# Kernel tuning notes

Measured on AMD Instinct MI355X. Metric: run time of the kernel, lower is better.

Reference implementation:

```python
import jax, jax.numpy as jnp
import numpy as np

DIM, D_STATE, D_CONV, EXPAND = 512, 16, 4, 2
D_INNER = EXPAND * DIM            # 1024
DT_RANK = (DIM + 15) // 16        # 32
B, L = 2, 2048


def setup_inputs() -> dict:
    key = jax.random.key(0)
    ks = jax.random.split(key, 12)
    s_in = 1.0 / np.sqrt(DIM)
    s_xp = 1.0 / np.sqrt(D_INNER)
    s_dt = 1.0 / np.sqrt(DT_RANK)
    return {
        "x": jax.random.normal(ks[0], (B, L, DIM), jnp.float32),
        "ln_g": jnp.ones((DIM,), jnp.float32),
        "ln_b": jnp.zeros((DIM,), jnp.float32),
        "W_in": jax.random.normal(ks[1], (2 * D_INNER, DIM), jnp.float32) * s_in,
        "conv_w": jax.random.normal(ks[2], (D_INNER, D_CONV), jnp.float32) * 0.5,
        "conv_b": jax.random.normal(ks[3], (D_INNER,), jnp.float32) * 0.1,
        "W_xproj": jax.random.normal(ks[4], (DT_RANK + 2 * D_STATE, D_INNER), jnp.float32) * s_xp,
        "W_dt": jax.random.normal(ks[5], (D_INNER, DT_RANK), jnp.float32) * s_dt,
        "b_dt": jax.random.normal(ks[6], (D_INNER,), jnp.float32) * 0.1 - 4.0,  # softplus -> small dt
        "A_log": jnp.log(jax.random.uniform(ks[7], (D_INNER, D_STATE), jnp.float32, 1.0, 16.0)),
        "Dp": jax.random.normal(ks[8], (D_INNER,), jnp.float32),
        "W_out": jax.random.normal(ks[9], (DIM, D_INNER), jnp.float32) * s_xp,
    }


def _layernorm(x, g, b, eps=1e-5):
    mu = jnp.mean(x, -1, keepdims=True)
    var = jnp.mean(jnp.square(x - mu), -1, keepdims=True)
    return (x - mu) * jax.lax.rsqrt(var + eps) * g + b


def reference(x, ln_g, ln_b, W_in, conv_w, conv_b, W_xproj, W_dt, b_dt, A_log, Dp, W_out):
    h = _layernorm(x, ln_g, ln_b)
    # input projection -> [B,L,2*d_inner]
    xz = jnp.einsum('bld,ed->ble', h, W_in)
    xp, z = jnp.split(xz, 2, axis=-1)
    # depthwise causal conv1d over time (kernel d_conv), then SiLU
    xp_pad = jnp.pad(xp, ((0, 0), (D_CONV - 1, 0), (0, 0)))
    xc = conv_b
    for k in range(D_CONV):
        xc = xc + xp_pad[:, k:k + L, :] * conv_w[:, k]
    xc = jax.nn.silu(xc)
    # x_proj -> dt, B, C
    proj = jnp.einsum('bld,ed->ble', xc, W_xproj)
    dt_r = proj[..., :DT_RANK]
    Bm = proj[..., DT_RANK:DT_RANK + D_STATE]          # [B,L,n]
    Cm = proj[..., DT_RANK + D_STATE:]                 # [B,L,n]
    dt = jax.nn.softplus(jnp.einsum('blr,dr->bld', dt_r, W_dt) + b_dt)  # [B,L,d]
    A = -jnp.exp(A_log)                                # [d,n]
    dA = jnp.exp(jnp.einsum('bld,dn->bldn', dt, A))    # [B,L,d,n]
    dBx = dt[..., None] * Bm[:, :, None, :] * xc[..., None]  # [B,L,d,n]
    # selective scan over time (time-major for lax.scan)
    def step(s, inp):
        dA_t, dBx_t, C_t = inp
        s = s * dA_t + dBx_t                           # [B,d,n]
        y_t = jnp.einsum('bdn,bn->bd', s, C_t)
        return s, y_t
    s0 = jnp.zeros((B, D_INNER, D_STATE), xc.dtype)
    _, ys = jax.lax.scan(step, s0,
                         (jnp.moveaxis(dA, 1, 0), jnp.moveaxis(dBx, 1, 0), jnp.moveaxis(Cm, 1, 0)))
    y = jnp.moveaxis(ys, 0, 1)                         # [B,L,d]
    y = y + xc * Dp
    y = y * jax.nn.silu(z)
    out = jnp.einsum('bld,ed->ble', y, W_out)
    return x + out  # dropout is identity in eval mode
```

## Files before the change

### kernel.cpp

```cpp
#include <hip/hip_runtime.h>
#include <hip/hip_bf16.h>
#include <math.h>

#define B_      2
#define L_      2048
#define DIM_    512
#define DINNER  1024
#define DTRANK  32
#define DSTATE  16
#define DCONV   4
#define BL      (B_ * L_)
#define NCHUNK  128
#define CBITS   7
#define CLEN    (L_ / NCHUNK)

typedef __attribute__((ext_vector_type(8))) short bf16x8;
typedef __attribute__((ext_vector_type(4))) float f32x4;

static __device__ __forceinline__ unsigned short f2bf(float f) {
  __hip_bfloat16 h = __float2bfloat16(f);
  return *(unsigned short*)&h;
}
static __device__ __forceinline__ float bf2f(unsigned short u) {
  return __uint_as_float(((unsigned int)u) << 16);
}

static __device__ __forceinline__ void gload16(const void* g, void* l) {
  __builtin_amdgcn_global_load_lds(
      (const __attribute__((address_space(1))) void*)g,
      (__attribute__((address_space(3))) void*)l, 16, 0, 0);
}

static __device__ __forceinline__ float softplus_f(float acc) {
  return (acc > 20.f) ? acc : __logf(1.f + __expf(acc));
}

__global__ __launch_bounds__(256) void cvt_ln_kernel(
    const float* __restrict__ s0, const float* __restrict__ s1,
    const float* __restrict__ s2, __hip_bfloat16* __restrict__ d0,
    __hip_bfloat16* __restrict__ d1, __hip_bfloat16* __restrict__ d2,
    const float* __restrict__ x, const float* __restrict__ g,
    const float* __restrict__ b, __hip_bfloat16* __restrict__ h) {
  int blk = blockIdx.x;
  if (blk < 1600) {
    int i = (blk * 256 + threadIdx.x) * 4;
    const float* s; __hip_bfloat16* d; int off;
    if (i < 1048576)            { s = s0; d = d0; off = i; }
    else if (i < 1048576+65536) { s = s1; d = d1; off = i - 1048576; }
    else                        { s = s2; d = d2; off = i - 1114112; }
    float4 v = *(const float4*)(s + off);
    d[off + 0] = __float2bfloat16(v.x);
    d[off + 1] = __float2bfloat16(v.y);
    d[off + 2] = __float2bfloat16(v.z);
    d[off + 3] = __float2bfloat16(v.w);
    return;
  }
  int row = (blk - 1600) * 4 + (threadIdx.x >> 6);
  int lane = threadIdx.x & 63;
  const float* xr = x + (size_t)row * DIM_;
  float v[8];
  float sum = 0.f;
#pragma unroll
  for (int i = 0; i < 8; i++) { v[i] = xr[lane + i * 64]; sum += v[i]; }
#pragma unroll
  for (int o = 32; o > 0; o >>= 1) sum += __shfl_xor(sum, o, 64);
  float mu = sum * (1.f / DIM_);
  float vs = 0.f;
#pragma unroll
  for (int i = 0; i < 8; i++) { float dd = v[i] - mu; vs += dd * dd; }
#pragma unroll
  for (int o = 32; o > 0; o >>= 1) vs += __shfl_xor(vs, o, 64);
  float rstd = rsqrtf(vs * (1.f / DIM_) + 1e-5f);
  __hip_bfloat16* hr = h + (size_t)row * DIM_;
#pragma unroll
  for (int i = 0; i < 8; i++) {
    int c = lane + i * 64;
    hr[c] = __float2bfloat16((v[i] - mu) * rstd * g[c] + b[c]);
  }
}

template <bool ADD_RES, bool OUT_BF16>
__global__ __launch_bounds__(256) void gemm_mfma_128(
    const __hip_bfloat16* __restrict__ A, int lda,
    const __hip_bfloat16* __restrict__ Bw, int ldb,
    const float* __restrict__ Res, int ldr,
    void* __restrict__ C, int ldc, int K) {
  __shared__ short As[128 * 64];
  __shared__ short Bs[128 * 64];
  int t = threadIdx.x;
  int n0 = blockIdx.x * 128, m0 = blockIdx.y * 128;
  int w = t >> 6, lane = t & 63;
  int wm = (w >> 1) * 64, wn = (w & 1) * 64;
  int l15 = lane & 15, quad = lane >> 4;
  int lr = lane >> 3, lc = (lane & 7) * 8;
  const short* Ag = (const short*)A + (size_t)(m0 + w * 32 + lr) * lda + lc;
  const short* Bg = (const short*)Bw + (size_t)(n0 + w * 32 + lr) * ldb + lc;
  f32x4 acc[4][4];
#pragma unroll
  for (int i = 0; i < 4; i++)
#pragma unroll
    for (int j = 0; j < 4; j++) acc[i][j] = (f32x4){0.f, 0.f, 0.f, 0.f};
  for (int k0 = 0; k0 < K; k0 += 64) {
    __syncthreads();
#pragma unroll
    for (int p = 0; p < 4; p++) {
      gload16(Ag + (size_t)(p * 8) * lda + k0, &As[(w * 32 + p * 8) * 64]);
      gload16(Bg + (size_t)(p * 8) * ldb + k0, &Bs[(w * 32 + p * 8) * 64]);
    }
    __syncthreads();
#pragma unroll
    for (int kk = 0; kk < 64; kk += 32) {
      bf16x8 af[4], bfr[4];
#pragma unroll
      for (int i = 0; i < 4; i++) {
        af[i] = *(const bf16x8*)&As[(wm + i * 16 + l15) * 64 + kk + quad * 8];
        bfr[i] = *(const bf16x8*)&Bs[(wn + i * 16 + l15) * 64 + kk + quad * 8];
      }
#pragma unroll
      for (int i = 0; i < 4; i++)
#pragma unroll
        for (int j = 0; j < 4; j++)
          acc[i][j] = __builtin_amdgcn_mfma_f32_16x16x32_bf16(
              af[i], bfr[j], acc[i][j], 0, 0, 0);
    }
  }
#pragma unroll
  for (int i = 0; i < 4; i++)
#pragma unroll
    for (int r = 0; r < 4; r++) {
      int row = m0 + wm + i * 16 + quad * 4 + r;
#pragma unroll
      for (int j = 0; j < 4; j++) {
        int col = n0 + wn + j * 16 + l15;
        float v = acc[i][j][r];
        if (ADD_RES) v += Res[(size_t)row * ldr + col];
        if (OUT_BF16)
          ((unsigned short*)C)[(size_t)row * ldc + col] = f2bf(v);
        else
          ((float*)C)[(size_t)row * ldc + col] = v;
      }
    }
}

template <bool ADD_RES>
__global__ __launch_bounds__(256) void gemm_mfma_64(
    const __hip_bfloat16* __restrict__ A, int lda,
    const __hip_bfloat16* __restrict__ Bw, int ldb,
    const float* __restrict__ Res, int ldr,
    float* __restrict__ C, int ldc, int K, size_t czs) {
  __shared__ short As[64 * 64];
  __shared__ short Bs[64 * 64];
  int t = threadIdx.x;
  int n0 = blockIdx.x * 64, m0 = blockIdx.y * 64;
  size_t kbase = (size_t)blockIdx.z * K;
  int w = t >> 6, lane = t & 63;
  int wm = (w >> 1) * 32, wn = (w & 1) * 32;
  int l15 = lane & 15, quad = lane >> 4;
  int lr = lane >> 3, lc = (lane & 7) * 8;
  const short* Ag = (const short*)A + (size_t)(m0 + w * 16 + lr) * lda + lc + kbase;
  const short* Bg = (const short*)Bw + (size_t)(n0 + w * 16 + lr) * ldb + lc + kbase;
  f32x4 acc[2][2];
#pragma unroll
  for (int i = 0; i < 2; i++)
#pragma unroll
    for (int j = 0; j < 2; j++) acc[i][j] = (f32x4){0.f, 0.f, 0.f, 0.f};
  for (int k0 = 0; k0 < K; k0 += 64) {
    __syncthreads();
#pragma unroll
    for (int p = 0; p < 2; p++) {
      gload16(Ag + (size_t)(p * 8) * lda + k0, &As[(w * 16 + p * 8) * 64]);
      gload16(Bg + (size_t)(p * 8) * ldb + k0, &Bs[(w * 16 + p * 8) * 64]);
    }
    __syncthreads();
#pragma unroll
    for (int kk = 0; kk < 64; kk += 32) {
      bf16x8 af[2], bfr[2];
#pragma unroll
      for (int i = 0; i < 2; i++) {
        af[i] = *(const bf16x8*)&As[(wm + i * 16 + l15) * 64 + kk + quad * 8];
        bfr[i] = *(const bf16x8*)&Bs[(wn + i * 16 + l15) * 64 + kk + quad * 8];
      }
#pragma unroll
      for (int i = 0; i < 2; i++)
#pragma unroll
        for (int j = 0; j < 2; j++)
          acc[i][j] = __builtin_amdgcn_mfma_f32_16x16x32_bf16(
              af[i], bfr[j], acc[i][j], 0, 0, 0);
    }
  }
  float* Cz = C + czs * blockIdx.z;
#pragma unroll
  for (int i = 0; i < 2; i++)
#pragma unroll
    for (int r = 0; r < 4; r++) {
      int row = m0 + wm + i * 16 + quad * 4 + r;
#pragma unroll
      for (int j = 0; j < 2; j++) {
        int col = n0 + wn + j * 16 + l15;
        float v = acc[i][j][r];
        if (ADD_RES) v += Res[(size_t)row * ldr + col];
        Cz[(size_t)row * ldc + col] = v;
      }
    }
}

__global__ __launch_bounds__(256) void gemm_proj_conv(
    const unsigned short* __restrict__ xzb,
    const __hip_bfloat16* __restrict__ Bw,
    const float* __restrict__ cw, const float* __restrict__ cb,
    __hip_bfloat16* __restrict__ xc_bf,
    float* __restrict__ C, size_t czs) {
  __shared__ short As[64 * 64];
  __shared__ short Bs[64 * 64];
  __shared__ float cws[256 * 4];
  __shared__ float cbs[256];
  int t = threadIdx.x;
  int m0 = blockIdx.y * 64;
  int kbase = blockIdx.z * 256;
  int w = t >> 6, lane = t & 63;
  int wm = (w >> 1) * 32, wn = (w & 1) * 32;
  int l15 = lane & 15, quad = lane >> 4;
  int lrB = lane >> 3, lcB = (lane & 7) * 8;
  const short* Bg = (const short*)Bw + (size_t)(w * 16 + lrB) * DINNER + lcB + kbase;
  *(float4*)&cws[t * 4] = *(const float4*)(cw + (size_t)(kbase + t) * 4);
  cbs[t] = cb[kbase + t];
  int ar = t >> 2, aq = t & 3;
  int bl = m0 + ar;
  int l = bl & (L_ - 1);
  f32x4 acc[2][2];
#pragma unroll
  for (int i = 0; i < 2; i++)
#pragma unroll
    for (int j = 0; j < 2; j++) acc[i][j] = (f32x4){0.f, 0.f, 0.f, 0.f};
  for (int k0 = 0; k0 < 256; k0 += 64) {
    __syncthreads();
#pragma unroll
    for (int p = 0; p < 2; p++)
      gload16(Bg + k0 + (size_t)(p * 8) * DINNER, &Bs[(w * 16 + p * 8) * 64]);
    int dl0 = k0 + aq * 16;
    const unsigned short* xrow = xzb + (size_t)bl * 2048 + kbase + dl0;
    float o[16];
#pragma unroll
    for (int cc = 0; cc < 16; cc++) o[cc] = cbs[dl0 + cc];
#pragma unroll
    for (int k = 0; k < 4; k++) {
      int off = 3 - k;
      bool ok = (l >= off);
      const unsigned short* src = xrow - (size_t)(ok ? off : 0) * 2048;
      bf16x8 v0 = *(const bf16x8*)(src);
      bf16x8 v1 = *(const bf16x8*)(src + 8);
#pragma unroll
      for (int cc = 0; cc < 8; cc++) {
        float xa = ok ? bf2f((unsigned short)v0[cc]) : 0.f;
        float xb = ok ? bf2f((unsigned short)v1[cc]) : 0.f;
        o[cc]     = fmaf(xa, cws[(dl0 + cc) * 4 + k], o[cc]);
        o[cc + 8] = fmaf(xb, cws[(dl0 + cc + 8) * 4 + k], o[cc + 8]);
      }
    }
    bf16x8 pa, pb;
#pragma unroll
    for (int cc = 0; cc < 8; cc++) {
      float va = o[cc] / (1.f + __expf(-o[cc]));
      float vb = o[cc + 8] / (1.f + __expf(-o[cc + 8]));
      pa[cc] = (short)f2bf(va);
      pb[cc] = (short)f2bf(vb);
    }
    *(bf16x8*)&As[ar * 64 + aq * 16] = pa;
    *(bf16x8*)&As[ar * 64 + aq * 16 + 8] = pb;
    unsigned short* xcd = (unsigned short*)xc_bf + (size_t)bl * DINNER + kbase + dl0;
    *(bf16x8*)xcd = pa;
    *(bf16x8*)(xcd + 8) = pb;
    __syncthreads();
#pragma unroll
    for (int kk = 0; kk < 64; kk += 32) {
      bf16x8 af[2], bfr[2];
#pragma unroll
      for (int i = 0; i < 2; i++) {
        af[i] = *(const bf16x8*)&As[(wm + i * 16 + l15) * 64 + kk + quad * 8];
        bfr[i] = *(const bf16x8*)&Bs[(wn + i * 16 + l15) * 64 + kk + quad * 8];
      }
#pragma unroll
      for (int i = 0; i < 2; i++)
#pragma unroll
        for (int j = 0; j < 2; j++)
          acc[i][j] = __builtin_amdgcn_mfma_f32_16x16x32_bf16(
              af[i], bfr[j], acc[i][j], 0, 0, 0);
    }
  }
  float* Cz = C + czs * blockIdx.z;
#pragma unroll
  for (int i = 0; i < 2; i++)
#pragma unroll
    for (int r = 0; r < 4; r++) {
      int row = m0 + wm + i * 16 + quad * 4 + r;
#pragma unroll
      for (int j = 0; j < 2; j++) {
        int col = wn + j * 16 + l15;
        Cz[(size_t)row * 64 + col] = acc[i][j][r];
      }
    }
}

__global__ __launch_bounds__(256) void dt_kernel(
    const float* __restrict__ pp, float* __restrict__ proj,
    const float* __restrict__ Wdt, const float* __restrict__ bdt,
    float* __restrict__ dt) {
  int blk = blockIdx.x;
  int dgrp = blk & 3;
  int bl0 = (blk >> 2) * 8;
  int tid = threadIdx.x;
  int d = dgrp * 256 + tid;
  __shared__ float pr[8 * 64];
  float w[32];
#pragma unroll
  for (int q = 0; q < 8; q++) {
    float4 wv = *(const float4*)(Wdt + (size_t)d * 32 + q * 4);
    w[q * 4 + 0] = wv.x; w[q * 4 + 1] = wv.y;
    w[q * 4 + 2] = wv.z; w[q * 4 + 3] = wv.w;
  }
  float bias = bdt[d];
  if (tid < 128) {
    int o4 = bl0 * 16 + tid;
    float4 v0 = ((const float4*)pp)[o4];
    float4 v1 = ((const float4*)pp)[o4 + 65536];
    float4 v2 = ((const float4*)pp)[o4 + 131072];
    float4 v3 = ((const float4*)pp)[o4 + 196608];
    float4 s;
    s.x = (v0.x + v1.x) + (v2.x + v3.x);
    s.y = (v0.y + v1.y) + (v2.y + v3.y);
    s.z = (v0.z + v1.z) + (v2.z + v3.z);
    s.w = (v0.w + v1.w) + (v2.w + v3.w);
    ((float4*)pr)[tid] = s;
    if (dgrp == 0) *(float4*)(proj + (size_t)bl0 * 64 + tid * 4) = s;
  }
  __syncthreads();
#pragma unroll
  for (int row = 0; row < 8; row++) {
    float a0 = 0.f, a1 = 0.f, a2 = 0.f, a3 = 0.f;
#pragma unroll
    for (int q = 0; q < 8; q++) {
      float4 pv = *(const float4*)&pr[row * 64 + q * 4];
      a0 = fmaf(pv.x, w[q * 4 + 0], a0);
      a1 = fmaf(pv.y, w[q * 4 + 1], a1);
      a2 = fmaf(pv.z, w[q * 4 + 2], a2);
      a3 = fmaf(pv.w, w[q * 4 + 3], a3);
    }
    float acc = bias + ((a0 + a1) + (a2 + a3));
    dt[(size_t)(bl0 + row) * DINNER + d] = softplus_f(acc);
  }
}

__global__ __launch_bounds__(256) void scan1_kernel(
    const float* __restrict__ dt, const __hip_bfloat16* __restrict__ xc_bf,
    const float* __restrict__ proj, const float* __restrict__ A_log,
    float* __restrict__ T, float* __restrict__ E) {
  int bid = blockIdx.x;
  int dgrp4 = bid & 15;
  int c = (bid >> 4) & (NCHUNK - 1);
  int b = bid >> (4 + CBITS);
  int tid = threadIdx.x;
  int dl = tid >> 2;
  int n4 = tid & 3;
  int d0 = dgrp4 * 64;
  int d = d0 + dl;
  int l0 = c * CLEN;
  __shared__ float dts[CLEN * 64];
  __shared__ float xcs[CLEN * 64];
  __shared__ float Bsh[CLEN * 16];
  {
    int row = tid >> 4, c4 = tid & 15;
    *(float4*)&dts[row * 64 + c4 * 4] =
        *(const float4*)(dt + (size_t)(b * L_ + l0 + row) * DINNER + d0 + c4 * 4);
  }
  if (tid < CLEN * 8) {
    int row = tid >> 3, c8 = tid & 7;
    bf16x8 v = *(const bf16x8*)((const unsigned short*)xc_bf +
                                (size_t)(b * L_ + l0 + row) * DINNER + d0 + c8 * 8);
#pragma unroll
    for (int k = 0; k < 8; k++)
      xcs[row * 64 + c8 * 8 + k] = bf2f((unsigned short)v[k]);
  }
  if (tid < CLEN * 4) {
    int row = tid >> 2, c4 = tid & 3;
    *(float4*)&Bsh[row * 16 + c4 * 4] =
        *(const float4*)(proj + (size_t)(b * L_ + l0 + row) * 64 + 32 + c4 * 4);
  }
  float4 av = *(const float4*)(A_log + (size_t)d * 16 + n4 * 4);
  float Aa[4] = {-__expf(av.x), -__expf(av.y), -__expf(av.z), -__expf(av.w)};
  __syncthreads();
  float Tn[4] = {1.f, 1.f, 1.f, 1.f};
  float En[4] = {0.f, 0.f, 0.f, 0.f};
#pragma unroll
  for (int l = 0; l < CLEN; l++) {
    float dtv = dts[l * 64 + dl];
    float dx = dtv * xcs[l * 64 + dl];
#pragma unroll
    for (int j = 0; j < 4; j++) {
      float dA = __expf(dtv * Aa[j]);
      Tn[j] *= dA;
      En[j] = En[j] * dA + dx * Bsh[l * 16 + n4 * 4 + j];
    }
  }
  size_t o = (((size_t)b * NCHUNK + c) * DINNER + d) * 16 + n4 * 4;
  *(float4*)&T[o] = *(float4*)Tn;
  *(float4*)&E[o] = *(float4*)En;
}

__global__ __launch_bounds__(256) void combine_kernel(
    float* __restrict__ T, const float* __restrict__ E) {
  int idx = blockIdx.x * 256 + threadIdx.x;
  int b = idx >> 14;
  int dn = idx & 16383;
  size_t base = (size_t)b * NCHUNK * (DINNER * 16) + dn;
  float s = 0.f;
#pragma unroll
  for (int batch = 0; batch < NCHUNK / 16; batch++) {
    float t[16], e[16];
#pragma unroll
    for (int j = 0; j < 16; j++) {
      size_t o = base + (size_t)(batch * 16 + j) * (DINNER * 16);
      t[j] = T[o]; e[j] = E[o];
    }
#pragma unroll
    for (int j = 0; j < 16; j++) {
      T[base + (size_t)(batch * 16 + j) * (DINNER * 16)] = s;
      s = t[j] * s + e[j];
    }
  }
}

__global__ __launch_bounds__(256) void scan2_kernel(
    const float* __restrict__ dt, const __hip_bfloat16* __restrict__ xc_bf,
    const float* __restrict__ proj, const float* __restrict__ A_log,
    const float* __restrict__ Sstart, const float* __restrict__ Dp,
    unsigned short* __restrict__ xzb) {
  int bid = blockIdx.x;
  int dgrp = bid & 3;
  int c = (bid >> 2) & (NCHUNK - 1);
  int b = bid >> (2 + CBITS);
  int tid = threadIdx.x;
  int d = dgrp * 256 + tid;
  int l0 = c * CLEN;
  __shared__ float Bsh[CLEN * 16];
  __shared__ float Csh[CLEN * 16];
  {
    int row = tid >> 4, nn = tid & 15;
    const float* pr = proj + (size_t)(b * L_ + l0 + row) * 64;
    Bsh[tid] = pr[32 + nn];
    Csh[tid] = pr[48 + nn];
  }
  float dtr[CLEN], xvr[CLEN];
  unsigned short zr[CLEN];
#pragma unroll
  for (int l = 0; l < CLEN; l++) {
    size_t bl = (size_t)(b * L_ + l0 + l);
    dtr[l] = dt[bl * DINNER + d];
    xvr[l] = __bfloat162float(xc_bf[bl * DINNER + d]);
    zr[l] = xzb[bl * 2048 + 1024 + d];
  }
  float Aa[16], s[16];
  size_t sb = (((size_t)b * NCHUNK + c) * DINNER + d) * 16;
#pragma unroll
  for (int q = 0; q < 4; q++) {
    float4 av = *(const float4*)(A_log + (size_t)d * 16 + q * 4);
    Aa[q * 4 + 0] = -__expf(av.x); Aa[q * 4 + 1] = -__expf(av.y);
    Aa[q * 4 + 2] = -__expf(av.z); Aa[q * 4 + 3] = -__expf(av.w);
    float4 sv = *(const float4*)(Sstart + sb + q * 4);
    s[q * 4 + 0] = sv.x; s[q * 4 + 1] = sv.y;
    s[q * 4 + 2] = sv.z; s[q * 4 + 3] = sv.w;
  }
  float Dv = Dp[d];
  __syncthreads();
#pragma unroll
  for (int l = 0; l < CLEN; l++) {
    float dtv = dtr[l];
    float xv = xvr[l];
    float dx = dtv * xv;
    float y = 0.f;
#pragma unroll
    for (int n = 0; n < 16; n++) {
      float dA = __expf(dtv * Aa[n]);
      s[n] = s[n] * dA + dx * Bsh[l * 16 + n];
      y += s[n] * Csh[l * 16 + n];
    }
    float zv = bf2f(zr[l]);
    float gate = zv / (1.f + __expf(-zv));
    xzb[(size_t)(b * L_ + l0 + l) * 2048 + d] = f2bf((y + xv * Dv) * gate);
  }
}

extern "C" void kernel_launch(void* const* d_in, const int* in_sizes, int n_in,
                              void* d_out, int out_size, void* d_ws, size_t ws_size,
                              hipStream_t stream) {
  const float* x      = (const float*)d_in[0];
  const float* ln_g   = (const float*)d_in[1];
  const float* ln_b   = (const float*)d_in[2];
  const float* W_in   = (const float*)d_in[3];
  const float* conv_w = (const float*)d_in[4];
  const float* conv_b = (const float*)d_in[5];
  const float* W_xprj = (const float*)d_in[6];
  const float* W_dt   = (const float*)d_in[7];
  const float* b_dt   = (const float*)d_in[8];
  const float* A_log  = (const float*)d_in[9];
  const float* Dp     = (const float*)d_in[10];
  const float* W_out  = (const float*)d_in[11];
  float* out = (float*)d_out;

  float* ws     = (float*)d_ws;
  float* xzb_f  = ws;
  float* xcbf_f = xzb_f + 4194304;
  float* proj   = xcbf_f + 2097152;
  float* pp     = proj + 262144;
  float* dtb    = pp + 1048576;
  float* T      = dtb + 4194304;
  float* E      = T + 4194304;
  float* hbf_f  = E + 4194304;
  float* wbf    = hbf_f + 1048576;

  unsigned short* xzb   = (unsigned short*)xzb_f;
  __hip_bfloat16* xc_bf = (__hip_bfloat16*)xcbf_f;
  __hip_bfloat16* h_bf  = (__hip_bfloat16*)hbf_f;
  __hip_bfloat16* Wb_in = (__hip_bfloat16*)wbf;
  __hip_bfloat16* Wb_xp = Wb_in + 1048576;
  __hip_bfloat16* Wb_out = Wb_xp + 65536;
  __hip_bfloat16* y_bf  = (__hip_bfloat16*)xzb;

  cvt_ln_kernel<<<1600 + BL / 4, 256, 0, stream>>>(
      W_in, W_xprj, W_out, Wb_in, Wb_xp, Wb_out, x, ln_g, ln_b, h_bf);
  gemm_mfma_128<false, true><<<dim3(2 * DINNER / 128, BL / 128), 256, 0, stream>>>(
      h_bf, DIM_, Wb_in, DIM_, nullptr, 0, xzb, 2 * DINNER, DIM_);
  gemm_proj_conv<<<dim3(1, BL / 64, 4), 256, 0, stream>>>(
      xzb, Wb_xp, conv_w, conv_b, xc_bf, pp, 262144);
  dt_kernel<<<(BL / 8) * 4, 256, 0, stream>>>(pp, proj, W_dt, b_dt, dtb);
  scan1_kernel<<<B_ * NCHUNK * 16, 256, 0, stream>>>(dtb, xc_bf, proj, A_log, T, E);
  combine_kernel<<<(B_ * DINNER * 16) / 256, 256, 0, stream>>>(T, E);
  scan2_kernel<<<B_ * NCHUNK * 4, 256, 0, stream>>>(dtb, xc_bf, proj, A_log, T, Dp, xzb);
  gemm_mfma_64<true><<<dim3(DIM_ / 64, BL / 64, 1), 256, 0, stream>>>(
      y_bf, 2048, Wb_out, DINNER, x, DIM_, out, DIM_, DINNER, 0);
}
```

Baseline: 192.7 us.

## Recompute dt inside both scan kernels instead of materializing dt buffer

Removes the standalone dt kernel that wrote a full [B,L,d_inner] fp32 dt tensor, and replaces it with a small reduction kernel that only sums the split-K partials into proj. Both scan1 and scan2 now recompute dt = softplus(dt_r·W_dt + b_dt) per chunk from the 32-wide dt_r in shared memory. This avoids writing and twice re-reading a 16 MB buffer, at the cost of duplicated dt arithmetic in both scan passes and extra register pressure in scan2.

After: 194.3 us. Within noise of the previous version (+0.8%).

```diff
diff --git a/kernel.cpp b/kernel.cpp
--- a/kernel.cpp
+++ b/kernel.cpp
@@ -301,79 +301,45 @@
     }
 }
 
-__global__ __launch_bounds__(256) void dt_kernel(
-    const float* __restrict__ pp, float* __restrict__ proj,
-    const float* __restrict__ Wdt, const float* __restrict__ bdt,
-    float* __restrict__ dt) {
-  int blk = blockIdx.x;
-  int dgrp = blk & 3;
-  int bl0 = (blk >> 2) * 8;
-  int tid = threadIdx.x;
-  int d = dgrp * 256 + tid;
-  __shared__ float pr[8 * 64];
-  float w[32];
-#pragma unroll
-  for (int q = 0; q < 8; q++) {
-    float4 wv = *(const float4*)(Wdt + (size_t)d * 32 + q * 4);
-    w[q * 4 + 0] = wv.x; w[q * 4 + 1] = wv.y;
-    w[q * 4 + 2] = wv.z; w[q * 4 + 3] = wv.w;
-  }
-  float bias = bdt[d];
-  if (tid < 128) {
-    int o4 = bl0 * 16 + tid;
-    float4 v0 = ((const float4*)pp)[o4];
-    float4 v1 = ((const float4*)pp)[o4 + 65536];
-    float4 v2 = ((const float4*)pp)[o4 + 131072];
-    float4 v3 = ((const float4*)pp)[o4 + 196608];
-    float4 s;
-    s.x = (v0.x + v1.x) + (v2.x + v3.x);
-    s.y = (v0.y + v1.y) + (v2.y + v3.y);
-    s.z = (v0.z + v1.z) + (v2.z + v3.z);
-    s.w = (v0.w + v1.w) + (v2.w + v3.w);
-    ((float4*)pr)[tid] = s;
-    if (dgrp == 0) *(float4*)(proj + (size_t)bl0 * 64 + tid * 4) = s;
-  }
-  __syncthreads();
-#pragma unroll
-  for (int row = 0; row < 8; row++) {
-    float a0 = 0.f, a1 = 0.f, a2 = 0.f, a3 = 0.f;
-#pragma unroll
-    for (int q = 0; q < 8; q++) {
-      float4 pv = *(const float4*)&pr[row * 64 + q * 4];
-      a0 = fmaf(pv.x, w[q * 4 + 0], a0);
-      a1 = fmaf(pv.y, w[q * 4 + 1], a1);
-      a2 = fmaf(pv.z, w[q * 4 + 2], a2);
-      a3 = fmaf(pv.w, w[q * 4 + 3], a3);
-    }
-    float acc = bias + ((a0 + a1) + (a2 + a3));
-    dt[(size_t)(bl0 + row) * DINNER + d] = softplus_f(acc);
-  }
+__global__ __launch_bounds__(256) void reduce4_kernel(
+    const float* __restrict__ pp, float* __restrict__ proj) {
+  int i4 = blockIdx.x * 256 + threadIdx.x;
+  float4 v0 = ((const float4*)pp)[i4];
+  float4 v1 = ((const float4*)pp)[i4 + 65536];
+  float4 v2 = ((const float4*)pp)[i4 + 131072];
+  float4 v3 = ((const float4*)pp)[i4 + 196608];
+  float4 s;
+  s.x = (v0.x + v1.x) + (v2.x + v3.x);
+  s.y = (v0.y + v1.y) + (v2.y + v3.y);
+  s.z = (v0.z + v1.z) + (v2.z + v3.z);
+  s.w = (v0.w + v1.w) + (v2.w + v3.w);
+  ((float4*)proj)[i4] = s;
 }
 
 __global__ __launch_bounds__(256) void scan1_kernel(
-    const float* __restrict__ dt, const __hip_bfloat16* __restrict__ xc_bf,
-    const float* __restrict__ proj, const float* __restrict__ A_log,
-    float* __restrict__ T, float* __restrict__ E) {
+    const __hip_bfloat16* __restrict__ xc_bf, const float* __restrict__ proj,
+    const float* __restrict__ A_log, const float* __restrict__ Wdt,
+    const float* __restrict__ bdt, float* __restrict__ T,
+    float* __restrict__ E) {
   int bid = blockIdx.x;
   int dgrp4 = bid & 15;
   int c = (bid >> 4) & (NCHUNK - 1);
   int b = bid >> (4 + CBITS);
   int tid = threadIdx.x;
-  int dl = tid >> 2;
-  int n4 = tid & 3;
   int d0 = dgrp4 * 64;
-  int d = d0 + dl;
   int l0 = c * CLEN;
   __shared__ float dts[CLEN * 64];
   __shared__ float xcs[CLEN * 64];
   __shared__ float Bsh[CLEN * 16];
-  {
-    int row = tid >> 4, c4 = tid & 15;
-    *(float4*)&dts[row * 64 + c4 * 4] =
-        *(const float4*)(dt + (size_t)(b * L_ + l0 + row) * DINNER + d0 + c4 * 4);
-  }
+  __shared__ float Pr[CLEN * 32];
   if (tid < CLEN * 8) {
-    int row = tid >> 3, c8 = tid & 7;
+    int row = tid >> 3, c4 = tid & 7;
+    *(float4*)&Pr[row * 32 + c4 * 4] =
+        *(const float4*)(proj + (size_t)(b * L_ + l0 + row) * 64 + c4 * 4);
+  }
+  if (tid >= 128) {
+    int t2 = tid - 128;
+    int row = t2 >> 3, c8 = t2 & 7;
     bf16x8 v = *(const bf16x8*)((const unsigned short*)xc_bf +
                                 (size_t)(b * L_ + l0 + row) * DINNER + d0 + c8 * 8);
 #pragma unroll
@@ -385,6 +351,34 @@
     *(float4*)&Bsh[row * 16 + c4 * 4] =
         *(const float4*)(proj + (size_t)(b * L_ + l0 + row) * 64 + 32 + c4 * 4);
   }
+  int dlc = tid & 63;
+  int row4 = tid >> 6;
+  float w[32];
+  const float* wr = Wdt + (size_t)(d0 + dlc) * 32;
+#pragma unroll
+  for (int q = 0; q < 8; q++) {
+    float4 wv = *(const float4*)(wr + q * 4);
+    w[q * 4 + 0] = wv.x; w[q * 4 + 1] = wv.y;
+    w[q * 4 + 2] = wv.z; w[q * 4 + 3] = wv.w;
+  }
+  float bias = bdt[d0 + dlc];
+  __syncthreads();
+#pragma unroll
+  for (int r = 0; r < 4; r++) {
+    int row = row4 * 4 + r;
+    float a0 = 0.f, a1 = 0.f, a2 = 0.f, a3 = 0.f;
+#pragma unroll
+    for (int q = 0; q < 8; q++) {
+      a0 = fmaf(Pr[row * 32 + q * 4 + 0], w[q * 4 + 0], a0);
+      a1 = fmaf(Pr[row * 32 + q * 4 + 1], w[q * 4 + 1], a1);
+      a2 = fmaf(Pr[row * 32 + q * 4 + 2], w[q * 4 + 2], a2);
+      a3 = fmaf(Pr[row * 32 + q * 4 + 3], w[q * 4 + 3], a3);
+    }
+    dts[row * 64 + dlc] = softplus_f(bias + ((a0 + a1) + (a2 + a3)));
+  }
+  int dl = tid >> 2;
+  int n4 = tid & 3;
+  int d = d0 + dl;
   float4 av = *(const float4*)(A_log + (size_t)d * 16 + n4 * 4);
   float Aa[4] = {-__expf(av.x), -__expf(av.y), -__expf(av.z), -__expf(av.w)};
   __syncthreads();
@@ -430,10 +424,10 @@
 }
 
 __global__ __launch_bounds__(256) void scan2_kernel(
-    const float* __restrict__ dt, const __hip_bfloat16* __restrict__ xc_bf,
-    const float* __restrict__ proj, const float* __restrict__ A_log,
-    const float* __restrict__ Sstart, const float* __restrict__ Dp,
-    unsigned short* __restrict__ xzb) {
+    const __hip_bfloat16* __restrict__ xc_bf, const float* __restrict__ proj,
+    const float* __restrict__ A_log, const float* __restrict__ Sstart,
+    const float* __restrict__ Dp, const float* __restrict__ Wdt,
+    const float* __restrict__ bdt, unsigned short* __restrict__ xzb) {
   int bid = blockIdx.x;
   int dgrp = bid & 3;
   int c = (bid >> 2) & (NCHUNK - 1);
@@ -443,18 +437,46 @@
   int l0 = c * CLEN;
   __shared__ float Bsh[CLEN * 16];
   __shared__ float Csh[CLEN * 16];
+  __shared__ float Pr[CLEN * 32];
   {
     int row = tid >> 4, nn = tid & 15;
     const float* pr = proj + (size_t)(b * L_ + l0 + row) * 64;
     Bsh[tid] = pr[32 + nn];
     Csh[tid] = pr[48 + nn];
   }
-  float dtr[CLEN], xvr[CLEN];
+  if (tid < CLEN * 8) {
+    int row = tid >> 3, c4 = tid & 7;
+    *(float4*)&Pr[row * 32 + c4 * 4] =
+        *(const float4*)(proj + (size_t)(b * L_ + l0 + row) * 64 + c4 * 4);
+  }
+  float w[32];
+  const float* wr = Wdt + (size_t)d * 32;
+#pragma unroll
+  for (int q = 0; q < 8; q++) {
+    float4 wv = *(const float4*)(wr + q * 4);
+    w[q * 4 + 0] = wv.x; w[q * 4 + 1] = wv.y;
+    w[q * 4 + 2] = wv.z; w[q * 4 + 3] = wv.w;
+  }
+  float bias = bdt[d];
+  __syncthreads();
+  float dt32[CLEN];
+#pragma unroll
+  for (int l = 0; l < CLEN; l++) {
+    float a0 = 0.f, a1 = 0.f, a2 = 0.f, a3 = 0.f;
+#pragma unroll
+    for (int q = 0; q < 8; q++) {
+      a0 = fmaf(Pr[l * 32 + q * 4 + 0], w[q * 4 + 0], a0);
+      a1 = fmaf(Pr[l * 32 + q * 4 + 1], w[q * 4 + 1], a1);
+      a2 = fmaf(Pr[l * 32 + q * 4 + 2], w[q * 4 + 2], a2);
+      a3 = fmaf(Pr[l * 32 + q * 4 + 3], w[q * 4 + 3], a3);
+    }
+    dt32[l] = softplus_f(bias + ((a0 + a1) + (a2 + a3)));
+  }
+  float xvr[CLEN];
   unsigned short zr[CLEN];
 #pragma unroll
   for (int l = 0; l < CLEN; l++) {
     size_t bl = (size_t)(b * L_ + l0 + l);
-    dtr[l] = dt[bl * DINNER + d];
     xvr[l] = __bfloat162float(xc_bf[bl * DINNER + d]);
     zr[l] = xzb[bl * 2048 + 1024 + d];
   }
@@ -470,10 +492,9 @@
     s[q * 4 + 2] = sv.z; s[q * 4 + 3] = sv.w;
   }
   float Dv = Dp[d];
-  __syncthreads();
 #pragma unroll
   for (int l = 0; l < CLEN; l++) {
-    float dtv = dtr[l];
+    float dtv = dt32[l];
     float xv = xvr[l];
     float dx = dtv * xv;
     float y = 0.f;
@@ -511,8 +532,7 @@
   float* xcbf_f = xzb_f + 4194304;
   float* proj   = xcbf_f + 2097152;
   float* pp     = proj + 262144;
-  float* dtb    = pp + 1048576;
-  float* T      = dtb + 4194304;
+  float* T      = pp + 1048576;
   float* E      = T + 4194304;
   float* hbf_f  = E + 4194304;
   float* wbf    = hbf_f + 1048576;
@@ -531,10 +551,12 @@
       h_bf, DIM_, Wb_in, DIM_, nullptr, 0, xzb, 2 * DINNER, DIM_);
   gemm_proj_conv<<<dim3(1, BL / 64, 4), 256, 0, stream>>>(
       xzb, Wb_xp, conv_w, conv_b, xc_bf, pp, 262144);
-  dt_kernel<<<(BL / 8) * 4, 256, 0, stream>>>(pp, proj, W_dt, b_dt, dtb);
-  scan1_kernel<<<B_ * NCHUNK * 16, 256, 0, stream>>>(dtb, xc_bf, proj, A_log, T, E);
+  reduce4_kernel<<<256, 256, 0, stream>>>(pp, proj);
+  scan1_kernel<<<B_ * NCHUNK * 16, 256, 0, stream>>>(
+      xc_bf, proj, A_log, W_dt, b_dt, T, E);
   combine_kernel<<<(B_ * DINNER * 16) / 256, 256, 0, stream>>>(T, E);
-  scan2_kernel<<<B_ * NCHUNK * 4, 256, 0, stream>>>(dtb, xc_bf, proj, A_log, T, Dp, xzb);
+  scan2_kernel<<<B_ * NCHUNK * 4, 256, 0, stream>>>(
+      xc_bf, proj, A_log, T, Dp, W_dt, b_dt, xzb);
   gemm_mfma_64<true><<<dim3(DIM_ / 64, BL / 64, 1), 256, 0, stream>>>(
       y_bf, 2048, Wb_out, DINNER, x, DIM_, out, DIM_, DINNER, 0);
 }
```
